# Kernel optimization log

Hardware: AMD Instinct MI355X
Metric: run time of the kernel (lower is better)

Reference implementation:

```python
import jax, jax.numpy as jnp
import numpy as np

G = 4          # num_groups == num_kv_groups


def _proj(W, b, xf):
    # 1x1 Conv3d == per-voxel linear: xf is [b, c, N]
    return jnp.einsum('oc,bcn->bon', W, xf) + b[None, :, None]


def setup_inputs() -> dict:
    key = jax.random.key(0)
    ks = jax.random.split(key, 5)
    c = 512
    x = jax.random.normal(ks[0], (2, c, 16, 16, 16), dtype=jnp.float32)
    s = 1.0 / np.sqrt(c)
    Wq = jax.random.normal(ks[1], (c, c), dtype=jnp.float32) * s
    Wk = jax.random.normal(ks[2], (c, c), dtype=jnp.float32) * s
    Wv = jax.random.normal(ks[3], (c, c), dtype=jnp.float32) * s
    Wo = jax.random.normal(ks[4], (c, c), dtype=jnp.float32) * s
    z = jnp.zeros((c,), dtype=jnp.float32)
    return {"x": x, "Wq": Wq, "bq": z, "Wk": Wk, "bk": z, "Wv": Wv, "bv": z, "Wo": Wo, "bo": z}


def reference(x, Wq, bq, Wk, bk, Wv, bv, Wo, bo):
    b, c, d, h, w = x.shape
    N = d * h * w
    gs = c // G                       # head (group) dim
    scale = gs ** -0.5
    xf = x.reshape(b, c, N)           # [b, c, N]
    q = _proj(Wq, bq, xf).reshape(b, G, gs, N).transpose(0, 1, 3, 2)  # [b,G,N,gs]
    k = _proj(Wk, bk, xf).reshape(b, G, gs, N).transpose(0, 1, 3, 2)
    v = _proj(Wv, bv, xf).reshape(b, G, gs, N).transpose(0, 1, 3, 2)
    sim = jnp.einsum('bgqd,bgkd->bgqk', q, k) * scale  # [b,G,N,N]
    attn = jax.nn.softmax(sim, axis=-1)
    out = jnp.einsum('bgqk,bgkd->bgqd', attn, v)       # [b,G,N,gs]
    out = out.transpose(0, 1, 3, 2).reshape(b, c, N)   # [b,c,N]
    out = _proj(Wo, bo, out).reshape(b, c, d, h, w)
    return x + out
```

## Files before the change

### kernel.cpp

```cpp
#include <hip/hip_runtime.h>
#include <hip/hip_bf16.h>
#include <stdint.h>

#define B_ 2
#define C_ 512
#define G_ 4
#define D_ 128
#define N_ 4096

typedef __bf16 bf16;
typedef __bf16 bf16x8 __attribute__((ext_vector_type(8)));
typedef float  f32x4  __attribute__((ext_vector_type(4)));
typedef float  f32x16 __attribute__((ext_vector_type(16)));

#define MFMA   __builtin_amdgcn_mfma_f32_16x16x32_bf16
#define MFMA32 __builtin_amdgcn_mfma_f32_32x32x16_bf16

#define SWZ(row, c) ((((c) ^ (((row) >> 1) & 3)) << 4))

#define OFF_Q   (0u)
#define OFF_K   (8388608u)
#define OFF_VT  (16777216u)
#define OFF_XT  (25165824u)
#define OFF_WB  (33554432u)
#define OFF_OP  (35651584u)
#define OFF_ML  (52428800u)
#define WS_NEED_SPLIT (52953088u)

__device__ inline unsigned pk2(float a, float b) {
    union { bf16 h[2]; unsigned u; } t;
    t.h[0] = (bf16)a; t.h[1] = (bf16)b;
    return t.u;
}
__device__ inline void pl32(unsigned &a, unsigned &b) {
    asm volatile("v_permlane32_swap_b32 %0, %1" : "+v"(a), "+v"(b));
}
__device__ inline void gload16(const char* src, char* lds) {
    __builtin_amdgcn_global_load_lds(
        (const __attribute__((address_space(1))) unsigned*)src,
        (__attribute__((address_space(3))) unsigned*)lds, 16, 0, 0);
}
__device__ inline float max3f(float a, float b, float c) {
    return fmaxf(fmaxf(a, b), c);
}

__global__ __launch_bounds__(256) void wcvt_kernel(const float* __restrict__ Wq,
                                                   const float* __restrict__ Wk,
                                                   const float* __restrict__ Wv,
                                                   const float* __restrict__ Wo,
                                                   bf16* __restrict__ out) {
    int m = blockIdx.y;
    const float* W = (m == 0) ? Wq : (m == 1) ? Wk : (m == 2) ? Wv : Wo;
    int i = (blockIdx.x * 256 + threadIdx.x) * 4;
    float4 v = *(const float4*)(W + i);
    union { bf16 h[4]; uint2 u; } pk;
    pk.h[0] = (bf16)v.x; pk.h[1] = (bf16)v.y; pk.h[2] = (bf16)v.z; pk.h[3] = (bf16)v.w;
    *(uint2*)(out + (size_t)m * (C_ * C_) + i) = pk.u;
}

__global__ __launch_bounds__(256) void xt_kernel(const float* __restrict__ x,
                                                 bf16* __restrict__ xT) {
    __shared__ bf16 t[64 * 80];
    int n0 = blockIdx.x * 64, c0 = blockIdx.y * 64, b = blockIdx.z;
    const float* xp = x + (size_t)b * C_ * N_;
#pragma unroll
    for (int i = 0; i < 16; ++i) {
        int idx = threadIdx.x + 256 * i;
        int cl = idx >> 6, nl = idx & 63;
        float v = xp[(size_t)(c0 + cl) * N_ + n0 + nl];
        t[nl * 80 + cl] = (bf16)v;
    }
    __syncthreads();
    bf16* xt = xT + ((size_t)b * N_ + n0) * C_ + c0;
#pragma unroll
    for (int i = 0; i < 2; ++i) {
        int id = threadIdx.x + 256 * i;
        int nl = id >> 3, c8 = (id & 7) * 8;
        *(uint4*)(xt + (size_t)nl * C_ + c8) = *(const uint4*)(t + nl * 80 + c8);
    }
}

__global__ __launch_bounds__(256) void qkv_kernel(const bf16* __restrict__ xT,
                                                  const bf16* __restrict__ WB,
                                                  const float* __restrict__ bq,
                                                  const float* __restrict__ bk,
                                                  const float* __restrict__ bv,
                                                  bf16* __restrict__ Q,
                                                  bf16* __restrict__ K,
                                                  bf16* __restrict__ Vt) {
    __shared__ char smem[32768];
    const int tid = threadIdx.x;
    const int w = tid >> 6, l = tid & 63;
    const int lr = l & 15, lg = l >> 4;
    const int wr = w >> 1, wc = w & 1;
    const int mat = blockIdx.z;
    const bf16* A = xT;
    const bf16* W = WB + (size_t)mat * (C_ * C_);
    const float* bias = (mat == 0) ? bq : (mat == 1) ? bk : bv;
    const int r0 = blockIdx.x * 128, o0 = blockIdx.y * 128;
    const float QSCALE = 0.08838834764831845f * 1.4426950408889634f;

    const char* srcA[2]; const char* srcB[2]; int dA[2], dB[2];
#pragma unroll
    for (int i = 0; i < 2; ++i) {
        int CL = tid + 256 * i, row = CL >> 2, c = CL & 3;
        srcA[i] = (const char*)(A + (size_t)(r0 + row) * C_) + SWZ(row, c);
        srcB[i] = (const char*)(W + (size_t)(o0 + row) * C_) + SWZ(row, c);
        dA[i] = CL << 4;
        dB[i] = 8192 + (CL << 4);
    }

    f32x4 z = {0.f, 0.f, 0.f, 0.f};
    f32x4 acc[4][4];
#pragma unroll
    for (int m = 0; m < 4; ++m)
#pragma unroll
        for (int n = 0; n < 4; ++n) acc[m][n] = z;

    auto STAGE = [&](int buf, int kt) {
        char* base = smem + buf * 16384;
        int kb = kt * 64;
#pragma unroll
        for (int i = 0; i < 2; ++i) {
            gload16(srcA[i] + kb, base + dA[i]);
            gload16(srcB[i] + kb, base + dB[i]);
        }
    };

    STAGE(0, 0);
    __syncthreads();
#pragma unroll 4
    for (int t = 0; t < 16; ++t) {
        int cur = t & 1;
        if (t < 15) STAGE(cur ^ 1, t + 1);
        char* Ab = smem + cur * 16384;
        char* Bb = Ab + 8192;
        bf16x8 af[4], bg_[4];
#pragma unroll
        for (int m = 0; m < 4; ++m) {
            int row = wr * 64 + m * 16 + lr;
            af[m] = *(const bf16x8*)(Ab + row * 64 + SWZ(row, lg));
        }
#pragma unroll
        for (int n = 0; n < 4; ++n) {
            int row = wc * 64 + n * 16 + lr;
            bg_[n] = *(const bf16x8*)(Bb + row * 64 + SWZ(row, lg));
        }
#pragma unroll
        for (int m = 0; m < 4; ++m)
#pragma unroll
            for (int n = 0; n < 4; ++n)
                acc[m][n] = MFMA(af[m], bg_[n], acc[m][n], 0, 0, 0);
        __syncthreads();
    }

#pragma unroll
    for (int n = 0; n < 4; ++n) {
        int o = o0 + wc * 64 + n * 16 + lr;
        float bs = bias[o];
        int g = o >> 7, d = o & 127;
#pragma unroll
        for (int m = 0; m < 4; ++m) {
            int row = r0 + wr * 64 + m * 16 + lg * 4;
            int b = row >> 12, nn = row & (N_ - 1);
            if (mat == 0) {
#pragma unroll
                for (int j = 0; j < 4; ++j)
                    Q[((size_t)(b * G_ + g) * N_ + nn + j) * D_ + d] =
                        (bf16)((acc[m][n][j] + bs) * QSCALE);
            } else if (mat == 1) {
#pragma unroll
                for (int j = 0; j < 4; ++j)
                    K[((size_t)(b * G_ + g) * N_ + nn + j) * D_ + d] =
                        (bf16)(acc[m][n][j] + bs);
            } else {
                union { bf16 h[4]; uint2 u; } pk;
#pragma unroll
                for (int j = 0; j < 4; ++j) pk.h[j] = (bf16)(acc[m][n][j] + bs);
                *(uint2*)(Vt + ((size_t)(b * G_ + g) * D_ + d) * N_ + nn) = pk.u;
            }
        }
    }
}

template<int SPLITS>
__global__ __launch_bounds__(512, 2) void attn_kernel(const bf16* __restrict__ Q,
                                                      const bf16* __restrict__ K,
                                                      const bf16* __restrict__ Vt,
                                                      bf16* __restrict__ XT,
                                                      bf16* __restrict__ Op,
                                                      float* __restrict__ ML) {
    __shared__ char smem[65536];
    const int tid = threadIdx.x;
    const int w = tid >> 6, l = tid & 63;
    const int l31 = l & 31, h = l >> 5;

    const int L = blockIdx.x;
    const int bg = L & 7;
    const int ix = L >> 3;
    const int sp = (SPLITS > 1) ? (ix >> 4) : 0;
    const int qb = (SPLITS > 1) ? (ix & 15) : ix;

    const bf16* Qh = Q + (size_t)bg * N_ * D_;
    const char* Kh = (const char*)(K + (size_t)bg * N_ * D_);
    const char* Vh = (const char*)(Vt + (size_t)bg * D_ * N_);
    const int q0 = qb * 256 + w * 32;
    const int kv0 = sp * (N_ / SPLITS);
    const int NT = N_ / SPLITS / 64;

    int offK[2], offV[2];
#pragma unroll
    for (int j = 0; j < 2; ++j) {
        int CL = (w * 2 + j) * 64 + l;
        int row = CL >> 4;
        int cp = (CL & 15) ^ (row & 15);
        offK[j] = row * 256 + cp * 16;
        int dv = 2 * row + (cp >> 3), k8 = cp & 7;
        offV[j] = dv * (N_ * 2) + k8 * 16;
    }

    bf16x8 aq[8];
#pragma unroll
    for (int kb = 0; kb < 8; ++kb)
        aq[kb] = *(const bf16x8*)(Qh + (size_t)(q0 + l31) * D_ + kb * 16 + h * 8);

    bf16 one_ = (bf16)1.0f;
    bf16x8 ones = {one_, one_, one_, one_, one_, one_, one_, one_};

    f32x16 oacc[4], lacc;
#pragma unroll
    for (int dt = 0; dt < 4; ++dt)
#pragma unroll
        for (int r = 0; r < 16; ++r) oacc[dt][r] = 0.f;
#pragma unroll
    for (int r = 0; r < 16; ++r) lacc[r] = 0.f;
    float mrun = -1e30f;
    const float THR = 5.0f;

    auto STAGE = [&](int buf, int kv) {
        const char* pk = Kh + (size_t)kv * 256;
        const char* pv = Vh + (size_t)kv * 2;
        char* kb = smem + buf * 32768 + w * 2048;
        char* vb = smem + buf * 32768 + 16384 + w * 2048;
#pragma unroll
        for (int j = 0; j < 2; ++j) gload16(pk + offK[j], kb + j * 1024);
#pragma unroll
        for (int j = 0; j < 2; ++j) gload16(pv + offV[j], vb + j * 1024);
    };

    STAGE(0, kv0);

    for (int t = 0; t < NT; ++t) {
        int cur = t & 1;
        __builtin_amdgcn_s_barrier();
        if (t + 1 < NT) {
            STAGE(cur ^ 1, kv0 + (t + 1) * 64);
            asm volatile("s_waitcnt vmcnt(4)" ::: "memory");
        } else {
            asm volatile("s_waitcnt vmcnt(0)" ::: "memory");
        }
        __builtin_amdgcn_sched_barrier(0);
        __builtin_amdgcn_s_barrier();
        char* Kb = smem + cur * 32768;
        char* Vb = smem + cur * 32768 + 16384;

        f32x16 s0, s1;
#pragma unroll
        for (int r = 0; r < 16; ++r) { s0[r] = 0.f; s1[r] = 0.f; }
        __builtin_amdgcn_s_setprio(1);
#pragma unroll
        for (int kb = 0; kb < 8; ++kb) {
            int ch = (((kb << 1) | h) ^ (l31 & 15)) << 4;
            bf16x8 kf0 = *(const bf16x8*)(Kb + (size_t)l31 * 256 + ch);
            s0 = MFMA32(kf0, aq[kb], s0, 0, 0, 0);
            bf16x8 kf1 = *(const bf16x8*)(Kb + (size_t)(32 + l31) * 256 + ch);
            s1 = MFMA32(kf1, aq[kb], s1, 0, 0, 0);
        }
        __builtin_amdgcn_s_setprio(0);

        float x0 = max3f(s0[0],  s0[1],  s0[2]);
        float x1 = max3f(s0[3],  s0[4],  s0[5]);
        float x2 = max3f(s0[6],  s0[7],  s0[8]);
        float x3 = max3f(s0[9],  s0[10], s0[11]);
        float x4 = max3f(s0[12], s0[13], s0[14]);
        float x5 = max3f(s0[15], s1[0],  s1[1]);
        float x6 = max3f(s1[2],  s1[3],  s1[4]);
        float x7 = max3f(s1[5],  s1[6],  s1[7]);
        float x8 = max3f(s1[8],  s1[9],  s1[10]);
        float x9 = max3f(s1[11], s1[12], s1[13]);
        float xa = fmaxf(s1[14], s1[15]);
        float y0 = max3f(x0, x1, x2);
        float y1 = max3f(x3, x4, x5);
        float y2 = max3f(x6, x7, x8);
        float y3 = fmaxf(x9, xa);
        float mt = fmaxf(max3f(y0, y1, y2), y3);
        mt = fmaxf(mt, __shfl_xor(mt, 32));

        if (__any(mt > mrun + THR)) {
            float mn = fmaxf(mrun, mt);
            float corr = __builtin_amdgcn_exp2f(mrun - mn);
            mrun = mn;
#pragma unroll
            for (int r = 0; r < 16; ++r) {
                int qr = (r & 3) + 8 * (r >> 2) + 4 * h;
                float cr = __shfl(corr, qr);
                lacc[r] *= cr;
#pragma unroll
                for (int dt = 0; dt < 4; ++dt) oacc[dt][r] *= cr;
            }
        }

#pragma unroll
        for (int r = 0; r < 16; ++r) {
            s0[r] = __builtin_amdgcn_exp2f(s0[r] - mrun);
            s1[r] = __builtin_amdgcn_exp2f(s1[r] - mrun);
        }

        bf16x8 pa0, pa1, pa2, pa3;
        {
            unsigned x0_ = pk2(s0[0], s0[1]),  y0_ = pk2(s0[4], s0[5]);  pl32(x0_, y0_);
            unsigned x1_ = pk2(s0[2], s0[3]),  y1_ = pk2(s0[6], s0[7]);  pl32(x1_, y1_);
            pa0 = __builtin_bit_cast(bf16x8, (uint4){x0_, x1_, y0_, y1_});
            unsigned x2_ = pk2(s0[8], s0[9]),  y2_ = pk2(s0[12], s0[13]); pl32(x2_, y2_);
            unsigned x3_ = pk2(s0[10], s0[11]), y3_ = pk2(s0[14], s0[15]); pl32(x3_, y3_);
            pa1 = __builtin_bit_cast(bf16x8, (uint4){x2_, x3_, y2_, y3_});
            unsigned x4_ = pk2(s1[0], s1[1]),  y4_ = pk2(s1[4], s1[5]);  pl32(x4_, y4_);
            unsigned x5_ = pk2(s1[2], s1[3]),  y5_ = pk2(s1[6], s1[7]);  pl32(x5_, y5_);
            pa2 = __builtin_bit_cast(bf16x8, (uint4){x4_, x5_, y4_, y5_});
            unsigned x6_ = pk2(s1[8], s1[9]),  y6_ = pk2(s1[12], s1[13]); pl32(x6_, y6_);
            unsigned x7_ = pk2(s1[10], s1[11]), y7_ = pk2(s1[14], s1[15]); pl32(x7_, y7_);
            pa3 = __builtin_bit_cast(bf16x8, (uint4){x6_, x7_, y6_, y7_});
        }

        __builtin_amdgcn_s_setprio(1);
#pragma unroll
        for (int sl = 0; sl < 4; ++sl) {
            bf16x8 pa = (sl == 0) ? pa0 : (sl == 1) ? pa1 : (sl == 2) ? pa2 : pa3;
#pragma unroll
            for (int dt = 0; dt < 4; ++dt) {
                int row = dt * 16 + (l31 >> 1);
                int ch = ((((l31 & 1) << 3) + (sl << 1) + h) ^ (l31 >> 1)) << 4;
                bf16x8 vf = *(const bf16x8*)(Vb + (size_t)row * 256 + ch);
                oacc[dt] = MFMA32(pa, vf, oacc[dt], 0, 0, 0);
            }
            lacc = MFMA32(pa, ones, lacc, 0, 0, 0);
        }
        __builtin_amdgcn_s_setprio(0);
    }

    if (SPLITS > 1) {
        float2* mlp = (float2*)ML + ((size_t)sp * 8 + bg) * N_ + q0;
#pragma unroll
        for (int r = 0; r < 16; ++r) {
            int qr = (r & 3) + 8 * (r >> 2) + 4 * h;
            float mv = __shfl(mrun, qr);
            if (l31 == 0) {
                float2 v; v.x = mv; v.y = lacc[r];
                mlp[qr] = v;
            }
        }
        bf16* op = Op + (((size_t)sp * 8 + bg) * N_ + q0) * D_;
#pragma unroll
        for (int dt = 0; dt < 4; ++dt)
#pragma unroll
            for (int r = 0; r < 16; ++r) {
                int qr = (r & 3) + 8 * (r >> 2) + 4 * h;
                op[(size_t)qr * D_ + dt * 32 + l31] = (bf16)oacc[dt][r];
            }
    } else {
        int b = bg >> 2, g = bg & 3;
#pragma unroll
        for (int r = 0; r < 16; ++r) {
            int qr = (r & 3) + 8 * (r >> 2) + 4 * h;
            float iv = 1.f / lacc[r];
#pragma unroll
            for (int dt = 0; dt < 4; ++dt)
                XT[((size_t)b * N_ + q0 + qr) * C_ + g * D_ + dt * 32 + l31] =
                    (bf16)(oacc[dt][r] * iv);
        }
    }
}

__global__ __launch_bounds__(256) void merge_kernel(const bf16* __restrict__ Op,
                                                    const float* __restrict__ ML,
                                                    bf16* __restrict__ XT) {
    int t = threadIdx.x & 15, rl = threadIdx.x >> 4;
    int r = blockIdx.x * 16 + rl;
    int bg = r >> 12, n = r & (N_ - 1);
    const float2* mlp = (const float2*)ML;
    float2 ml0 = mlp[r], ml1 = mlp[32768 + r];
    float mm = fmaxf(ml0.x, ml1.x);
    float w0 = __builtin_amdgcn_exp2f(ml0.x - mm);
    float w1 = __builtin_amdgcn_exp2f(ml1.x - mm);
    float inv = 1.f / (w0 * ml0.y + w1 * ml1.y);
    w0 *= inv; w1 *= inv;
    bf16x8 o0 = *(const bf16x8*)(Op + (size_t)r * D_ + t * 8);
    bf16x8 o1 = *(const bf16x8*)(Op + (size_t)(32768 + r) * D_ + t * 8);
    union { bf16 h[8]; uint4 u; } pk;
#pragma unroll
    for (int e = 0; e < 8; ++e)
        pk.h[e] = (bf16)(w0 * (float)o0[e] + w1 * (float)o1[e]);
    int b = bg >> 2, g = bg & 3;
    *(uint4*)(XT + ((size_t)b * N_ + n) * C_ + g * D_ + t * 8) = pk.u;
}

__global__ __launch_bounds__(256) void oproj_kernel(const bf16* __restrict__ Ob,
                                                    const bf16* __restrict__ WB,
                                                    const float* __restrict__ bo,
                                                    const float* __restrict__ x,
                                                    float* __restrict__ out) {
    __shared__ char smem[24576];
    const int tid = threadIdx.x;
    const int w = tid >> 6, l = tid & 63;
    const int lr = l & 15, lg = l >> 4;
    const int wr = w >> 1, wc = w & 1;
    const bf16* W = WB + (size_t)3 * (C_ * C_);
    const int r0 = blockIdx.x * 128, o0 = blockIdx.y * 64;

    const char* srcA[2]; int dA[2];
#pragma unroll
    for (int i = 0; i < 2; ++i) {
        int CL = tid + 256 * i, row = CL >> 2, c = CL & 3;
        srcA[i] = (const char*)(Ob + (size_t)(r0 + row) * C_) + SWZ(row, c);
        dA[i] = CL << 4;
    }
    const char* srcB; int dB;
    {
        int CL = tid, row = CL >> 2, c = CL & 3;
        srcB = (const char*)(W + (size_t)(o0 + row) * C_) + SWZ(row, c);
        dB = 8192 + (CL << 4);
    }

    f32x4 z = {0.f, 0.f, 0.f, 0.f};
    f32x4 acc[4][2];
#pragma unroll
    for (int m = 0; m < 4; ++m) { acc[m][0] = z; acc[m][1] = z; }

    auto STAGE = [&](int buf, int kt) {
        char* base = smem + buf * 12288;
        int kb = kt * 64;
#pragma unroll
        for (int i = 0; i < 2; ++i) gload16(srcA[i] + kb, base + dA[i]);
        gload16(srcB + kb, base + dB);
    };

    STAGE(0, 0);
    __syncthreads();
#pragma unroll 4
    for (int t = 0; t < 16; ++t) {
        int cur = t & 1;
        if (t < 15) STAGE(cur ^ 1, t + 1);
        char* Ab = smem + cur * 12288;
        char* Bb = Ab + 8192;
        bf16x8 af[4], bg_[2];
#pragma unroll
        for (int m = 0; m < 4; ++m) {
            int row = wr * 64 + m * 16 + lr;
            af[m] = *(const bf16x8*)(Ab + row * 64 + SWZ(row, lg));
        }
#pragma unroll
        for (int n = 0; n < 2; ++n) {
            int row = wc * 32 + n * 16 + lr;
            bg_[n] = *(const bf16x8*)(Bb + row * 64 + SWZ(row, lg));
        }
#pragma unroll
        for (int m = 0; m < 4; ++m)
#pragma unroll
            for (int n = 0; n < 2; ++n)
                acc[m][n] = MFMA(af[m], bg_[n], acc[m][n], 0, 0, 0);
        __syncthreads();
    }

#pragma unroll
    for (int n = 0; n < 2; ++n) {
        int o = o0 + wc * 32 + n * 16 + lr;
        float bs = bo[o];
#pragma unroll
        for (int m = 0; m < 4; ++m) {
            int row = r0 + wr * 64 + m * 16 + lg * 4;
            int b = row >> 12, nn = row & (N_ - 1);
            size_t base = ((size_t)b * C_ + o) * N_ + nn;
            float4 xv = *(const float4*)(x + base);
            float4 ov;
            ov.x = acc[m][n][0] + bs + xv.x;
            ov.y = acc[m][n][1] + bs + xv.y;
            ov.z = acc[m][n][2] + bs + xv.z;
            ov.w = acc[m][n][3] + bs + xv.w;
            *(float4*)(out + base) = ov;
        }
    }
}

extern "C" void kernel_launch(void* const* d_in, const int* in_sizes, int n_in,
                              void* d_out, int out_size, void* d_ws, size_t ws_size,
                              hipStream_t stream) {
    const float* x  = (const float*)d_in[0];
    const float* Wq = (const float*)d_in[1];
    const float* bq = (const float*)d_in[2];
    const float* Wk = (const float*)d_in[3];
    const float* bk = (const float*)d_in[4];
    const float* Wv = (const float*)d_in[5];
    const float* bv = (const float*)d_in[6];
    const float* Wo = (const float*)d_in[7];
    const float* bo = (const float*)d_in[8];

    char* ws = (char*)d_ws;
    bf16* Q   = (bf16*)(ws + OFF_Q);
    bf16* K   = (bf16*)(ws + OFF_K);
    bf16* Vt  = (bf16*)(ws + OFF_VT);
    bf16* XT  = (bf16*)(ws + OFF_XT);
    bf16* WB  = (bf16*)(ws + OFF_WB);
    bf16* Op  = (bf16*)(ws + OFF_OP);
    float* ML = (float*)(ws + OFF_ML);
    float* out = (float*)d_out;

    hipLaunchKernelGGL(wcvt_kernel, dim3(256, 4), dim3(256), 0, stream, Wq, Wk, Wv, Wo, WB);
    hipLaunchKernelGGL(xt_kernel, dim3(64, 8, 2), dim3(256), 0, stream, x, XT);
    hipLaunchKernelGGL(qkv_kernel, dim3(64, 4, 3), dim3(256), 0, stream,
                       XT, WB, bq, bk, bv, Q, K, Vt);
    if (ws_size >= (size_t)WS_NEED_SPLIT) {
        hipLaunchKernelGGL(attn_kernel<2>, dim3(256), dim3(512), 0, stream,
                           Q, K, Vt, XT, Op, ML);
        hipLaunchKernelGGL(merge_kernel, dim3(2048), dim3(256), 0, stream, Op, ML, XT);
    } else {
        hipLaunchKernelGGL(attn_kernel<1>, dim3(128), dim3(512), 0, stream,
                           Q, K, Vt, XT, Op, ML);
    }
    hipLaunchKernelGGL(oproj_kernel, dim3(64, 8), dim3(256), 0, stream, XT, WB, bo, x, out);
}
```

Baseline: 132.9 us.

## Load K tiles straight into registers and stage only V through LDS

The attention kernel stops staging K through shared memory. Each wave now loads its K fragments directly from global memory into double-buffered register arrays, while V is still double-buffered in LDS at half the previous footprint. The loop is unrolled by two so the register buffers can ping-pong. The aim is to drop LDS traffic and LDS capacity for K, but every wave now fetches the whole K tile redundantly. The 128 extra VGPRs for K buffers risk spilling under the 512×2 launch bound.

```diff
diff --git a/kernel.cpp b/kernel.cpp
--- a/kernel.cpp
+++ b/kernel.cpp
@@ -190,7 +190,7 @@
                                                       bf16* __restrict__ XT,
                                                       bf16* __restrict__ Op,
                                                       float* __restrict__ ML) {
-    __shared__ char smem[65536];
+    __shared__ char smem[32768];
     const int tid = threadIdx.x;
     const int w = tid >> 6, l = tid & 63;
     const int l31 = l & 31, h = l >> 5;
@@ -208,13 +208,12 @@
     const int kv0 = sp * (N_ / SPLITS);
     const int NT = N_ / SPLITS / 64;
 
-    int offK[2], offV[2];
+    int offV[2];
 #pragma unroll
     for (int j = 0; j < 2; ++j) {
         int CL = (w * 2 + j) * 64 + l;
         int row = CL >> 4;
         int cp = (CL & 15) ^ (row & 15);
-        offK[j] = row * 256 + cp * 16;
         int dv = 2 * row + (cp >> 3), k8 = cp & 7;
         offV[j] = dv * (N_ * 2) + k8 * 16;
     }
@@ -237,116 +236,110 @@
     float mrun = -1e30f;
     const float THR = 5.0f;
 
-    auto STAGE = [&](int buf, int kv) {
-        const char* pk = Kh + (size_t)kv * 256;
+    auto STAGE_V = [&](int buf, int kv) {
         const char* pv = Vh + (size_t)kv * 2;
-        char* kb = smem + buf * 32768 + w * 2048;
-        char* vb = smem + buf * 32768 + 16384 + w * 2048;
-#pragma unroll
-        for (int j = 0; j < 2; ++j) gload16(pk + offK[j], kb + j * 1024);
+        char* vb = smem + buf * 16384 + w * 2048;
 #pragma unroll
         for (int j = 0; j < 2; ++j) gload16(pv + offV[j], vb + j * 1024);
     };
 
-    STAGE(0, kv0);
-
-    for (int t = 0; t < NT; ++t) {
-        int cur = t & 1;
-        __builtin_amdgcn_s_barrier();
-        if (t + 1 < NT) {
-            STAGE(cur ^ 1, kv0 + (t + 1) * 64);
-            asm volatile("s_waitcnt vmcnt(4)" ::: "memory");
-        } else {
-            asm volatile("s_waitcnt vmcnt(0)" ::: "memory");
-        }
-        __builtin_amdgcn_sched_barrier(0);
-        __builtin_amdgcn_s_barrier();
-        char* Kb = smem + cur * 32768;
-        char* Vb = smem + cur * 32768 + 16384;
-
-        f32x16 s0, s1;
-#pragma unroll
-        for (int r = 0; r < 16; ++r) { s0[r] = 0.f; s1[r] = 0.f; }
-        __builtin_amdgcn_s_setprio(1);
-#pragma unroll
-        for (int kb = 0; kb < 8; ++kb) {
-            int ch = (((kb << 1) | h) ^ (l31 & 15)) << 4;
-            bf16x8 kf0 = *(const bf16x8*)(Kb + (size_t)l31 * 256 + ch);
-            s0 = MFMA32(kf0, aq[kb], s0, 0, 0, 0);
-            bf16x8 kf1 = *(const bf16x8*)(Kb + (size_t)(32 + l31) * 256 + ch);
-            s1 = MFMA32(kf1, aq[kb], s1, 0, 0, 0);
-        }
-        __builtin_amdgcn_s_setprio(0);
-
-        float x0 = max3f(s0[0],  s0[1],  s0[2]);
-        float x1 = max3f(s0[3],  s0[4],  s0[5]);
-        float x2 = max3f(s0[6],  s0[7],  s0[8]);
-        float x3 = max3f(s0[9],  s0[10], s0[11]);
-        float x4 = max3f(s0[12], s0[13], s0[14]);
-        float x5 = max3f(s0[15], s1[0],  s1[1]);
-        float x6 = max3f(s1[2],  s1[3],  s1[4]);
-        float x7 = max3f(s1[5],  s1[6],  s1[7]);
-        float x8 = max3f(s1[8],  s1[9],  s1[10]);
-        float x9 = max3f(s1[11], s1[12], s1[13]);
-        float xa = fmaxf(s1[14], s1[15]);
-        float y0 = max3f(x0, x1, x2);
-        float y1 = max3f(x3, x4, x5);
-        float y2 = max3f(x6, x7, x8);
-        float y3 = fmaxf(x9, xa);
-        float mt = fmaxf(max3f(y0, y1, y2), y3);
-        mt = fmaxf(mt, __shfl_xor(mt, 32));
-
-        if (__any(mt > mrun + THR)) {
-            float mn = fmaxf(mrun, mt);
-            float corr = __builtin_amdgcn_exp2f(mrun - mn);
-            mrun = mn;
-#pragma unroll
-            for (int r = 0; r < 16; ++r) {
-                int qr = (r & 3) + 8 * (r >> 2) + 4 * h;
-                float cr = __shfl(corr, qr);
-                lacc[r] *= cr;
-#pragma unroll
-                for (int dt = 0; dt < 4; ++dt) oacc[dt][r] *= cr;
-            }
-        }
-
-#pragma unroll
-        for (int r = 0; r < 16; ++r) {
-            s0[r] = __builtin_amdgcn_exp2f(s0[r] - mrun);
-            s1[r] = __builtin_amdgcn_exp2f(s1[r] - mrun);
-        }
-
-        bf16x8 pa0, pa1, pa2, pa3;
-        {
-            unsigned x0_ = pk2(s0[0], s0[1]),  y0_ = pk2(s0[4], s0[5]);  pl32(x0_, y0_);
-            unsigned x1_ = pk2(s0[2], s0[3]),  y1_ = pk2(s0[6], s0[7]);  pl32(x1_, y1_);
-            pa0 = __builtin_bit_cast(bf16x8, (uint4){x0_, x1_, y0_, y1_});
-            unsigned x2_ = pk2(s0[8], s0[9]),  y2_ = pk2(s0[12], s0[13]); pl32(x2_, y2_);
-            unsigned x3_ = pk2(s0[10], s0[11]), y3_ = pk2(s0[14], s0[15]); pl32(x3_, y3_);
-            pa1 = __builtin_bit_cast(bf16x8, (uint4){x2_, x3_, y2_, y3_});
-            unsigned x4_ = pk2(s1[0], s1[1]),  y4_ = pk2(s1[4], s1[5]);  pl32(x4_, y4_);
-            unsigned x5_ = pk2(s1[2], s1[3]),  y5_ = pk2(s1[6], s1[7]);  pl32(x5_, y5_);
-            pa2 = __builtin_bit_cast(bf16x8, (uint4){x4_, x5_, y4_, y5_});
-            unsigned x6_ = pk2(s1[8], s1[9]),  y6_ = pk2(s1[12], s1[13]); pl32(x6_, y6_);
-            unsigned x7_ = pk2(s1[10], s1[11]), y7_ = pk2(s1[14], s1[15]); pl32(x7_, y7_);
-            pa3 = __builtin_bit_cast(bf16x8, (uint4){x6_, x7_, y6_, y7_});
-        }
-
-        __builtin_amdgcn_s_setprio(1);
-#pragma unroll
-        for (int sl = 0; sl < 4; ++sl) {
-            bf16x8 pa = (sl == 0) ? pa0 : (sl == 1) ? pa1 : (sl == 2) ? pa2 : pa3;
-#pragma unroll
-            for (int dt = 0; dt < 4; ++dt) {
-                int row = dt * 16 + (l31 >> 1);
-                int ch = ((((l31 & 1) << 3) + (sl << 1) + h) ^ (l31 >> 1)) << 4;
-                bf16x8 vf = *(const bf16x8*)(Vb + (size_t)row * 256 + ch);
-                oacc[dt] = MFMA32(pa, vf, oacc[dt], 0, 0, 0);
-            }
-            lacc = MFMA32(pa, ones, lacc, 0, 0, 0);
-        }
-        __builtin_amdgcn_s_setprio(0);
-    }
+    bf16x8 kA0[8], kA1[8], kB0[8], kB1[8];
+
+#define LOADK(D0, D1, kvv)                                                        \
+    _Pragma("unroll")                                                             \
+    for (int kb = 0; kb < 8; ++kb) {                                              \
+        D0[kb] = *(const bf16x8*)(Kh + (size_t)(kvv + l31) * 256 + (((kb << 1) | h) << 4));       \
+        D1[kb] = *(const bf16x8*)(Kh + (size_t)(kvv + 32 + l31) * 256 + (((kb << 1) | h) << 4));  \
+    }
+
+    STAGE_V(0, kv0);
+    LOADK(kA0, kA1, kv0)
+
+#define BODY(KC0, KC1, KN0, KN1, P, T)                                            \
+    {                                                                             \
+        const int t_ = (T);                                                       \
+        asm volatile("s_waitcnt vmcnt(16)" ::: "memory");     \
+        __builtin_amdgcn_sched_barrier(0);                                        \
+        __builtin_amdgcn_s_barrier();                           \
+        if (t_ + 1 < NT) STAGE_V((P) ^ 1, kv0 + (t_ + 1) * 64);                   \
+        if (t_ + 1 < NT) { LOADK(KN0, KN1, (kv0 + (t_ + 1) * 64)) }               \
+        __builtin_amdgcn_sched_barrier(0);                                        \
+        f32x16 s0, s1;                                                            \
+        _Pragma("unroll") for (int r = 0; r < 16; ++r) { s0[r] = 0.f; s1[r] = 0.f; } \
+        __builtin_amdgcn_s_setprio(1);                                            \
+        _Pragma("unroll") for (int kb = 0; kb < 8; ++kb) {                        \
+            s0 = MFMA32(KC0[kb], aq[kb], s0, 0, 0, 0);                            \
+            s1 = MFMA32(KC1[kb], aq[kb], s1, 0, 0, 0);                            \
+        }                                                                         \
+        __builtin_amdgcn_s_setprio(0);                                            \
+        float x0 = max3f(s0[0],  s0[1],  s0[2]);                                  \
+        float x1 = max3f(s0[3],  s0[4],  s0[5]);                                  \
+        float x2 = max3f(s0[6],  s0[7],  s0[8]);                                  \
+        float x3 = max3f(s0[9],  s0[10], s0[11]);                                 \
+        float x4 = max3f(s0[12], s0[13], s0[14]);                                 \
+        float x5 = max3f(s0[15], s1[0],  s1[1]);                                  \
+        float x6 = max3f(s1[2],  s1[3],  s1[4]);                                  \
+        float x7 = max3f(s1[5],  s1[6],  s1[7]);                                  \
+        float x8 = max3f(s1[8],  s1[9],  s1[10]);                                 \
+        float x9 = max3f(s1[11], s1[12], s1[13]);                                 \
+        float xa = fmaxf(s1[14], s1[15]);                                         \
+        float y0 = max3f(x0, x1, x2);                                             \
+        float y1 = max3f(x3, x4, x5);                                             \
+        float y2 = max3f(x6, x7, x8);                                             \
+        float y3 = fmaxf(x9, xa);                                                 \
+        float mt = fmaxf(max3f(y0, y1, y2), y3);                                  \
+        mt = fmaxf(mt, __shfl_xor(mt, 32));                                       \
+        if (__any(mt > mrun + THR)) {                                             \
+            float mn = fmaxf(mrun, mt);                                           \
+            float corr = __builtin_amdgcn_exp2f(mrun - mn);                       \
+            mrun = mn;                                                            \
+            _Pragma("unroll") for (int r = 0; r < 16; ++r) {                      \
+                int qr = (r & 3) + 8 * (r >> 2) + 4 * h;                          \
+                float cr = __shfl(corr, qr);                                      \
+                lacc[r] *= cr;                                                    \
+                _Pragma("unroll") for (int dt = 0; dt < 4; ++dt) oacc[dt][r] *= cr; \
+            }                                                                     \
+        }                                                                         \
+        _Pragma("unroll") for (int r = 0; r < 16; ++r) {                          \
+            s0[r] = __builtin_amdgcn_exp2f(s0[r] - mrun);                         \
+            s1[r] = __builtin_amdgcn_exp2f(s1[r] - mrun);                         \
+        }                                                                         \
+        bf16x8 pa0, pa1, pa2, pa3;                                                \
+        {                                                                         \
+            unsigned u0 = pk2(s0[0], s0[1]),  v0 = pk2(s0[4], s0[5]);  pl32(u0, v0); \
+            unsigned u1 = pk2(s0[2], s0[3]),  v1 = pk2(s0[6], s0[7]);  pl32(u1, v1); \
+            pa0 = __builtin_bit_cast(bf16x8, (uint4){u0, u1, v0, v1});            \
+            unsigned u2 = pk2(s0[8], s0[9]),  v2 = pk2(s0[12], s0[13]); pl32(u2, v2); \
+            unsigned u3 = pk2(s0[10], s0[11]), v3 = pk2(s0[14], s0[15]); pl32(u3, v3); \
+            pa1 = __builtin_bit_cast(bf16x8, (uint4){u2, u3, v2, v3});            \
+            unsigned u4 = pk2(s1[0], s1[1]),  v4 = pk2(s1[4], s1[5]);  pl32(u4, v4); \
+            unsigned u5 = pk2(s1[2], s1[3]),  v5 = pk2(s1[6], s1[7]);  pl32(u5, v5); \
+            pa2 = __builtin_bit_cast(bf16x8, (uint4){u4, u5, v4, v5});            \
+            unsigned u6 = pk2(s1[8], s1[9]),  v6 = pk2(s1[12], s1[13]); pl32(u6, v6); \
+            unsigned u7 = pk2(s1[10], s1[11]), v7 = pk2(s1[14], s1[15]); pl32(u7, v7); \
+            pa3 = __builtin_bit_cast(bf16x8, (uint4){u6, u7, v6, v7});            \
+        }                                                                         \
+        char* Vb = smem + (P) * 16384;                                            \
+        __builtin_amdgcn_s_setprio(1);                                            \
+        _Pragma("unroll") for (int sl = 0; sl < 4; ++sl) {                        \
+            bf16x8 pa = (sl == 0) ? pa0 : (sl == 1) ? pa1 : (sl == 2) ? pa2 : pa3; \
+            _Pragma("unroll") for (int dt = 0; dt < 4; ++dt) {                    \
+                int row = dt * 16 + (l31 >> 1);                                   \
+                int ch = ((((l31 & 1) << 3) + (sl << 1) + h) ^ (l31 >> 1)) << 4;  \
+                bf16x8 vf = *(const bf16x8*)(Vb + (size_t)row * 256 + ch);        \
+                oacc[dt] = MFMA32(pa, vf, oacc[dt], 0, 0, 0);                     \
+            }                                                                     \
+            lacc = MFMA32(pa, ones, lacc, 0, 0, 0);                               \
+        }                                                                         \
+        __builtin_amdgcn_s_setprio(0);                                            \
+    }
+
+    for (int t2 = 0; t2 < NT; t2 += 2) {
+        BODY(kA0, kA1, kB0, kB1, 0, t2)
+        BODY(kB0, kB1, kA0, kA1, 1, t2 + 1)
+    }
+#undef BODY
+#undef LOADK
 
     if (SPLITS > 1) {
         float2* mlp = (float2*)ML + ((size_t)sp * 8 + bg) * N_ + q0;
```

After: 290.6 us. 119% more time.

## Fuse split-KV merge into output projection A-tile staging

Applied to the files above, without the earlier changes.

Removes the separate merge kernel and folds the two-split softmax combine into the output-projection GEMM. Each block computes per-row, per-group merge weights from ML up front. It then loads both partial outputs into registers, blends them, and writes the bf16 result into the swizzled LDS tile after the MFMAs for the current stage. This saves one launch and the XT write/read round trip. In exchange, every one of the 8 column blocks re-reads both partial buffers (redundant traffic), the A loads become synchronous register loads instead of direct-to-LDS, and register pressure rises.

```diff
diff --git a/kernel.cpp b/kernel.cpp
--- a/kernel.cpp
+++ b/kernel.cpp
@@ -381,30 +381,10 @@
     }
 }
 
-__global__ __launch_bounds__(256) void merge_kernel(const bf16* __restrict__ Op,
+template<int FUSE>
+__global__ __launch_bounds__(256) void oproj_kernel(const bf16* __restrict__ Ob,
+                                                    const bf16* __restrict__ Op,
                                                     const float* __restrict__ ML,
-                                                    bf16* __restrict__ XT) {
-    int t = threadIdx.x & 15, rl = threadIdx.x >> 4;
-    int r = blockIdx.x * 16 + rl;
-    int bg = r >> 12, n = r & (N_ - 1);
-    const float2* mlp = (const float2*)ML;
-    float2 ml0 = mlp[r], ml1 = mlp[32768 + r];
-    float mm = fmaxf(ml0.x, ml1.x);
-    float w0 = __builtin_amdgcn_exp2f(ml0.x - mm);
-    float w1 = __builtin_amdgcn_exp2f(ml1.x - mm);
-    float inv = 1.f / (w0 * ml0.y + w1 * ml1.y);
-    w0 *= inv; w1 *= inv;
-    bf16x8 o0 = *(const bf16x8*)(Op + (size_t)r * D_ + t * 8);
-    bf16x8 o1 = *(const bf16x8*)(Op + (size_t)(32768 + r) * D_ + t * 8);
-    union { bf16 h[8]; uint4 u; } pk;
-#pragma unroll
-    for (int e = 0; e < 8; ++e)
-        pk.h[e] = (bf16)(w0 * (float)o0[e] + w1 * (float)o1[e]);
-    int b = bg >> 2, g = bg & 3;
-    *(uint4*)(XT + ((size_t)b * N_ + n) * C_ + g * D_ + t * 8) = pk.u;
-}
-
-__global__ __launch_bounds__(256) void oproj_kernel(const bf16* __restrict__ Ob,
                                                     const bf16* __restrict__ WB,
                                                     const float* __restrict__ bo,
                                                     const float* __restrict__ x,
@@ -417,12 +397,32 @@
     const bf16* W = WB + (size_t)3 * (C_ * C_);
     const int r0 = blockIdx.x * 128, o0 = blockIdx.y * 64;
 
-    const char* srcA[2]; int dA[2];
+    const char* srcA[2]; int dA[2], cpw[2]; size_t opRow[2];
+    float w0f[2][4], w1f[2][4];
 #pragma unroll
     for (int i = 0; i < 2; ++i) {
         int CL = tid + 256 * i, row = CL >> 2, c = CL & 3;
-        srcA[i] = (const char*)(Ob + (size_t)(r0 + row) * C_) + SWZ(row, c);
+        cpw[i] = c ^ ((row >> 1) & 3);
         dA[i] = CL << 4;
+        srcA[i] = (const char*)(Ob + (size_t)(r0 + row) * C_) + (cpw[i] << 4);
+        if (FUSE) {
+            int rg = r0 + row;
+            int b = rg >> 12, n = rg & (N_ - 1);
+            const float2* mlp = (const float2*)ML;
+#pragma unroll
+            for (int g = 0; g < 4; ++g) {
+                int bg = b * 4 + g;
+                float2 ml0 = mlp[(size_t)bg * N_ + n];
+                float2 ml1 = mlp[(size_t)(8 + bg) * N_ + n];
+                float mm = fmaxf(ml0.x, ml1.x);
+                float a0 = __builtin_amdgcn_exp2f(ml0.x - mm);
+                float a1 = __builtin_amdgcn_exp2f(ml1.x - mm);
+                float inv = 1.f / (a0 * ml0.y + a1 * ml1.y);
+                w0f[i][g] = a0 * inv;
+                w1f[i][g] = a1 * inv;
+            }
+            opRow[i] = ((size_t)(b * 4) * N_ + n) * 256u;
+        }
     }
     const char* srcB; int dB;
     {
@@ -436,20 +436,51 @@
 #pragma unroll
     for (int m = 0; m < 4; ++m) { acc[m][0] = z; acc[m][1] = z; }
 
-    auto STAGE = [&](int buf, int kt) {
+    uint4 a0r[2], a1r[2];
+    auto LOAD_A = [&](int kt) {
+        int g = kt >> 2;
+#pragma unroll
+        for (int i = 0; i < 2; ++i) {
+            size_t off = opRow[i] + (size_t)g * ((size_t)N_ * 256u - 256u)
+                       + (size_t)(kt * 64) + ((size_t)cpw[i] << 4);
+            a0r[i] = *(const uint4*)((const char*)Op + off);
+            a1r[i] = *(const uint4*)((const char*)Op + 8388608u + off);
+        }
+    };
+    auto WRITE_A = [&](int buf, int kt) {
+        int g = kt >> 2;
         char* base = smem + buf * 12288;
-        int kb = kt * 64;
-#pragma unroll
-        for (int i = 0; i < 2; ++i) gload16(srcA[i] + kb, base + dA[i]);
-        gload16(srcB + kb, base + dB);
+#pragma unroll
+        for (int i = 0; i < 2; ++i) {
+            union { uint4 u; bf16 h[8]; } u0, u1, uo;
+            u0.u = a0r[i]; u1.u = a1r[i];
+#pragma unroll
+            for (int e = 0; e < 8; ++e)
+                uo.h[e] = (bf16)(w0f[i][g] * (float)u0.h[e] + w1f[i][g] * (float)u1.h[e]);
+            *(uint4*)(base + dA[i]) = uo.u;
+        }
     };
-
-    STAGE(0, 0);
+    auto STAGE_A_PLAIN = [&](int buf, int kt) {
+        char* base = smem + buf * 12288;
+#pragma unroll
+        for (int i = 0; i < 2; ++i) gload16(srcA[i] + kt * 64, base + dA[i]);
+    };
+    auto STAGE_B = [&](int buf, int kt) {
+        gload16(srcB + kt * 64, smem + buf * 12288 + dB);
+    };
+
+    STAGE_B(0, 0);
+    if (FUSE) { LOAD_A(0); WRITE_A(0, 0); }
+    else       STAGE_A_PLAIN(0, 0);
     __syncthreads();
-#pragma unroll 4
+
     for (int t = 0; t < 16; ++t) {
         int cur = t & 1;
-        if (t < 15) STAGE(cur ^ 1, t + 1);
+        if (t < 15) {
+            STAGE_B(cur ^ 1, t + 1);
+            if (FUSE) LOAD_A(t + 1);
+            else      STAGE_A_PLAIN(cur ^ 1, t + 1);
+        }
         char* Ab = smem + cur * 12288;
         char* Bb = Ab + 8192;
         bf16x8 af[4], bg_[2];
@@ -468,6 +499,7 @@
 #pragma unroll
             for (int n = 0; n < 2; ++n)
                 acc[m][n] = MFMA(af[m], bg_[n], acc[m][n], 0, 0, 0);
+        if (FUSE && t < 15) WRITE_A(cur ^ 1, t + 1);
         __syncthreads();
     }
 
@@ -521,10 +553,12 @@
     if (ws_size >= (size_t)WS_NEED_SPLIT) {
         hipLaunchKernelGGL(attn_kernel<2>, dim3(256), dim3(512), 0, stream,
                            Q, K, Vt, XT, Op, ML);
-        hipLaunchKernelGGL(merge_kernel, dim3(2048), dim3(256), 0, stream, Op, ML, XT);
+        hipLaunchKernelGGL(oproj_kernel<1>, dim3(64, 8), dim3(256), 0, stream,
+                           XT, Op, ML, WB, bo, x, out);
     } else {
         hipLaunchKernelGGL(attn_kernel<1>, dim3(128), dim3(512), 0, stream,
                            Q, K, Vt, XT, Op, ML);
-    }
-    hipLaunchKernelGGL(oproj_kernel, dim3(64, 8), dim3(256), 0, stream, XT, WB, bo, x, out);
-}
+        hipLaunchKernelGGL(oproj_kernel<0>, dim3(64, 8), dim3(256), 0, stream,
+                           XT, Op, ML, WB, bo, x, out);
+    }
+}
```

Result: no change. 131.9 us (-0.7%).
